# Kernel tuning notes

Measured on AMD Instinct MI355X. Metric: run time of the kernel, lower is better.

Reference implementation:

```python
import jax, jax.numpy as jnp
import numpy as np

B, NPTS = 32, 2048          # batch, raw points per cloud
G, M = 128, 32              # num_group (FPS centers), group_size (KNN)
C, DEPTH, H = 384, 12, 8    # trans_dim, depth, num_heads
HD = C // H                 # head_dim = 48, divisible by 6 for 3-axis RoPE
MLP = 4 * C
CLS = 40
THETA = 100.0


def _ln(x, g, b):
    m = x.mean(-1, keepdims=True)
    v = ((x - m) ** 2).mean(-1, keepdims=True)
    return (x - m) * jax.lax.rsqrt(v + 1e-5) * g + b


def _rot_pairs(x, cos, sin):
    # rotate consecutive (even, odd) pairs of the last dim by angle arrays
    x2 = x.reshape(x.shape[:-1] + (-1, 2))
    xr, xi = x2[..., 0], x2[..., 1]
    return jnp.stack([xr * cos - xi * sin, xr * sin + xi * cos], -1).reshape(x.shape)


def _fps(pts, n):
    # farthest point sampling, first point = index 0
    Bb, N, _ = pts.shape

    def step(carry, _):
        dist, last = carry
        lp = jnp.take_along_axis(pts, last[:, None, None], axis=1)  # (B,1,3)
        dist = jnp.minimum(dist, jnp.sum((pts - lp) ** 2, -1))
        nxt = jnp.argmax(dist, -1).astype(jnp.int32)
        return (dist, nxt), last

    init = (jnp.full((Bb, N), 1e10, pts.dtype), jnp.zeros((Bb,), jnp.int32))
    _, idxs = jax.lax.scan(step, init, None, length=n)
    return idxs.T  # (B, n)


def forward(pts, enc_w1, enc_b1, enc_g1, enc_be1, enc_w2, enc_b2,
            enc_w3, enc_b3, enc_g2, enc_be2, enc_w4, enc_b4,
            cls_token, cls_pos,
            ln1_g, ln1_b, qkv_w, givens_theta, proj_w, proj_b,
            ln2_g, ln2_b, fc1_w, fc1_b, fc2_w, fc2_b,
            norm_g, norm_b,
            hw1, hb1, hg1, hbe1, hw2, hb2, hg2, hbe2, hw3, hb3):
    # ---- Group divider: FPS centers + KNN neighborhoods ----
    cidx = _fps(pts, G)
    center = jnp.take_along_axis(pts, cidx[:, :, None], axis=1)          # (B,G,3)
    d2 = jnp.sum((center[:, :, None, :] - pts[:, None, :, :]) ** 2, -1)  # (B,G,N)
    _, kidx = jax.lax.top_k(-d2, M)                                      # (B,G,M)
    neigh = jax.vmap(lambda p, i: p[i])(pts, kidx) - center[:, :, None, :]

    # ---- mini-PointNet encoder (BN in eval mode: running mean 0, var 1) ----
    x = neigh.reshape(B * G, M, 3)
    f = jax.nn.relu((x @ enc_w1.T + enc_b1) * enc_g1 + enc_be1)          # (BG,M,128)
    f = f @ enc_w2.T + enc_b2                                            # (BG,M,256)
    fg = jnp.max(f, 1, keepdims=True)
    f = jnp.concatenate([jnp.broadcast_to(fg, f.shape), f], -1)          # (BG,M,512)
    f = jax.nn.relu((f @ enc_w3.T + enc_b3) * enc_g2 + enc_be2)
    f = f @ enc_w4.T + enc_b4                                            # (BG,M,C)
    tok = jnp.max(f, 1).reshape(B, G, C)

    # ---- 3-axis axial RoPE frequencies from group centers ----
    nfr = HD // 6
    fr = 1.0 / (THETA ** (jnp.arange(nfr, dtype=pts.dtype) * 2.0 / (HD // 3)))
    ang = (center[..., None] * fr).reshape(B, G, 3 * nfr)                # (B,G,HD/2)
    pcos, psin = jnp.cos(ang)[:, None], jnp.sin(ang)[:, None]            # (B,1,G,HD/2)

    # ---- tokens: [CLS | groups] ----
    x = jnp.concatenate([jnp.broadcast_to(cls_token + cls_pos, (B, 1, C)), tok], 1)
    N = G + 1
    scale = HD ** -0.5

    for i in range(DEPTH):
        h = _ln(x, ln1_g[i], ln1_b[i])
        qkv = (h @ qkv_w[i].T).reshape(B, N, 3, H, HD).transpose(2, 0, 3, 1, 4)
        q, k, v = qkv[0], qkv[1], qkv[2]                                 # (B,H,N,HD)
        # learnable Givens rotation (per-head block-diagonal pair rotations)
        gcos = jnp.cos(givens_theta[i])[None, :, None]                   # (1,H,1,HD/2)
        gsin = jnp.sin(givens_theta[i])[None, :, None]
        q = _rot_pairs(q, gcos, gsin)
        k = _rot_pairs(k, gcos, gsin)
        # positional RoPE on non-CLS tokens only
        q = jnp.concatenate([q[:, :, :1], _rot_pairs(q[:, :, 1:], pcos, psin)], 2)
        k = jnp.concatenate([k[:, :, :1], _rot_pairs(k[:, :, 1:], pcos, psin)], 2)
        attn = jax.nn.softmax(jnp.einsum('bhqd,bhkd->bhqk', q, k) * scale, -1)
        o = jnp.einsum('bhqk,bhkd->bhqd', attn, v).transpose(0, 2, 1, 3).reshape(B, N, C)
        x = x + o @ proj_w[i].T + proj_b[i]
        h = _ln(x, ln2_g[i], ln2_b[i])
        x = x + jax.nn.gelu(h @ fc1_w[i].T + fc1_b[i], approximate=False) @ fc2_w[i].T + fc2_b[i]

    x = _ln(x, norm_g, norm_b)
    feat = jnp.concatenate([x[:, 0], jnp.max(x[:, 1:], 1)], -1)          # (B,2C)
    hfe = jax.nn.relu((feat @ hw1.T + hb1) * hg1 + hbe1)
    hfe = jax.nn.relu((hfe @ hw2.T + hb2) * hg2 + hbe2)
    return hfe @ hw3.T + hb3                                             # (B,CLS)


def setup_inputs() -> dict:
    key = jax.random.key(0)
    ks = iter(jax.random.split(key, 64))
    nrm = lambda *s: jax.random.normal(next(ks), s, jnp.float32) * 0.02
    d = dict(
        pts=jax.random.normal(next(ks), (B, NPTS, 3), jnp.float32),
        enc_w1=nrm(128, 3), enc_b1=jnp.zeros(128), enc_g1=jnp.ones(128), enc_be1=jnp.zeros(128),
        enc_w2=nrm(256, 128), enc_b2=jnp.zeros(256),
        enc_w3=nrm(512, 512), enc_b3=jnp.zeros(512), enc_g2=jnp.ones(512), enc_be2=jnp.zeros(512),
        enc_w4=nrm(C, 512), enc_b4=jnp.zeros(C),
        cls_token=nrm(1, 1, C), cls_pos=nrm(1, 1, C),
        ln1_g=jnp.ones((DEPTH, C)), ln1_b=jnp.zeros((DEPTH, C)),
        qkv_w=nrm(DEPTH, 3 * C, C), givens_theta=nrm(DEPTH, H, HD // 2),
        proj_w=nrm(DEPTH, C, C), proj_b=jnp.zeros((DEPTH, C)),
        ln2_g=jnp.ones((DEPTH, C)), ln2_b=jnp.zeros((DEPTH, C)),
        fc1_w=nrm(DEPTH, MLP, C), fc1_b=jnp.zeros((DEPTH, MLP)),
        fc2_w=nrm(DEPTH, C, MLP), fc2_b=jnp.zeros((DEPTH, C)),
        norm_g=jnp.ones(C), norm_b=jnp.zeros(C),
        hw1=nrm(256, 2 * C), hb1=jnp.zeros(256), hg1=jnp.ones(256), hbe1=jnp.zeros(256),
        hw2=nrm(256, 256), hb2=jnp.zeros(256), hg2=jnp.ones(256), hbe2=jnp.zeros(256),
        hw3=nrm(CLS, 256), hb3=jnp.zeros(CLS),
    )
    return d


def reference(pts, enc_w1, enc_b1, enc_g1, enc_be1, enc_w2, enc_b2,
              enc_w3, enc_b3, enc_g2, enc_be2, enc_w4, enc_b4,
              cls_token, cls_pos,
              ln1_g, ln1_b, qkv_w, givens_theta, proj_w, proj_b,
              ln2_g, ln2_b, fc1_w, fc1_b, fc2_w, fc2_b,
              norm_g, norm_b,
              hw1, hb1, hg1, hbe1, hw2, hb2, hg2, hbe2, hw3, hb3):
    return forward(pts, enc_w1, enc_b1, enc_g1, enc_be1, enc_w2, enc_b2,
                   enc_w3, enc_b3, enc_g2, enc_be2, enc_w4, enc_b4,
                   cls_token, cls_pos,
                   ln1_g, ln1_b, qkv_w, givens_theta, proj_w, proj_b,
                   ln2_g, ln2_b, fc1_w, fc1_b, fc2_w, fc2_b,
                   norm_g, norm_b,
                   hw1, hb1, hg1, hbe1, hw2, hb2, hg2, hbe2, hw3, hb3)
```

## Files before the change

kernel.cpp:

```cpp
#include <hip/hip_runtime.h>
#include <math.h>

constexpr int kB   = 32;
constexpr int kN   = 2048;
constexpr int kG   = 128;
constexpr int kM   = 32;
constexpr int kC   = 384;
constexpr int kH   = 8;
constexpr int kHD  = 48;
constexpr int kNT  = 129;
constexpr int kMLP = 1536;
constexpr int kRows = kB * kNT;
constexpr int kGC  = 512;
constexpr int kRC  = kGC * kM;

typedef __attribute__((ext_vector_type(8))) short bf16x8;
typedef __attribute__((ext_vector_type(4))) float f32x4;

__device__ __forceinline__ unsigned short f2bf(float x) {
  unsigned u = __float_as_uint(x);
  unsigned r = (u + 0x7fffu + ((u >> 16) & 1u)) >> 16;
  return (unsigned short)r;
}
__device__ __forceinline__ float bf2f(unsigned short u) {
  return __uint_as_float(((unsigned)u) << 16);
}

__global__ __launch_bounds__(64) void fps_kernel(
    const float* __restrict__ pts, float* __restrict__ center)
{
  #pragma clang fp contract(off)
  __shared__ float sx[kN], sy[kN], sz[kN];
  const int b = blockIdx.x, lane = threadIdx.x;
  const float* P = pts + (size_t)b * kN * 3;
  float rx[32], ry[32], rz[32], rd[32];
  const int base = lane * 32;
  #pragma unroll
  for (int j = 0; j < 32; ++j) {
    int i = base + j;
    float x = P[3*i], y = P[3*i+1], z = P[3*i+2];
    rx[j] = x; ry[j] = y; rz[j] = z; rd[j] = 1e10f;
    sx[i] = x; sy[i] = y; sz[i] = z;
  }
  __syncthreads();
  int last = 0;
  float* cb = center + (size_t)b * kG * 3;
  for (int it = 0; it < kG; ++it) {
    float lx = sx[last], ly = sy[last], lz = sz[last];
    if (lane == 0) { cb[3*it] = lx; cb[3*it+1] = ly; cb[3*it+2] = lz; }
    float bestv = -1.0f; int besti = kN;
    #pragma unroll
    for (int j = 0; j < 32; ++j) {
      float dx = rx[j]-lx, dy = ry[j]-ly, dz = rz[j]-lz;
      float d = (dx*dx + dy*dy) + dz*dz;
      float nd = fminf(rd[j], d);
      rd[j] = nd;
      if (nd > bestv) { bestv = nd; besti = base + j; }
    }
    #pragma unroll
    for (int off = 1; off < 64; off <<= 1) {
      float vv = __shfl_xor(bestv, off);
      int   ii = __shfl_xor(besti, off);
      if (vv > bestv || (vv == bestv && ii < besti)) { bestv = vv; besti = ii; }
    }
    last = besti;
  }
}

__global__ void rope_kernel(const float* __restrict__ center,
                            float* __restrict__ pcs, float* __restrict__ psn)
{
  int idx = blockIdx.x*256 + threadIdx.x;
  if (idx >= kB*kG*24) return;
  int p  = idx % 24;
  int bg = idx / 24;
  int axis = p >> 3, j = p & 7;
  float e  = (float)(2*j) / 16.0f;
  float fr = 1.0f / powf(100.0f, e);
  float ang = center[(size_t)bg*3 + axis] * fr;
  pcs[idx] = cosf(ang);
  psn[idx] = sinf(ang);
}

__global__ __launch_bounds__(256) void knn_kernel(
    const float* __restrict__ pts, const float* __restrict__ center,
    float* __restrict__ neigh)
{
  #pragma clang fp contract(off)
  __shared__ float d2s[kN];
  __shared__ float rv[4];
  __shared__ int   ri[4];
  const int t = threadIdx.x;
  const int bg = blockIdx.x;
  const int b = bg >> 7;
  const float* P = pts + (size_t)b * kN * 3;
  const float cx = center[(size_t)bg*3+0];
  const float cy = center[(size_t)bg*3+1];
  const float cz = center[(size_t)bg*3+2];
  for (int i = t; i < kN; i += 256) {
    float dx = cx - P[3*i], dy = cy - P[3*i+1], dz = cz - P[3*i+2];
    d2s[i] = (dx*dx + dy*dy) + dz*dz;
  }
  __syncthreads();
  for (int m = 0; m < kM; ++m) {
    float bestv = 3.0e38f; int besti = kN;
    for (int i = t; i < kN; i += 256) {
      float v = d2s[i];
      if (v < bestv || (v == bestv && i < besti)) { bestv = v; besti = i; }
    }
    #pragma unroll
    for (int off = 32; off > 0; off >>= 1) {
      float vv = __shfl_down(bestv, off);
      int   ii = __shfl_down(besti, off);
      if (vv < bestv || (vv == bestv && ii < besti)) { bestv = vv; besti = ii; }
    }
    if ((t & 63) == 0) { rv[t>>6] = bestv; ri[t>>6] = besti; }
    __syncthreads();
    if (t == 0) {
      float bv = rv[0]; int bi = ri[0];
      for (int w = 1; w < 4; ++w)
        if (rv[w] < bv || (rv[w] == bv && ri[w] < bi)) { bv = rv[w]; bi = ri[w]; }
      d2s[bi] = 3.0e38f;
      float* o = neigh + ((size_t)bg*kM + m)*3;
      o[0] = P[3*bi+0] - cx; o[1] = P[3*bi+1] - cy; o[2] = P[3*bi+2] - cz;
    }
    __syncthreads();
  }
}

__global__ __launch_bounds__(256) void enc1_kernel(
    const float* __restrict__ neighC,
    const float* __restrict__ w1, const float* __restrict__ b1,
    const float* __restrict__ g1, const float* __restrict__ be1,
    unsigned short* __restrict__ f1c)
{
  const int t = threadIdx.x;
  const int r = blockIdx.x*2 + (t >> 7);
  const int c = t & 127;
  const float* nr = neighC + (size_t)r*3;
  float x0 = nr[0], x1 = nr[1], x2 = nr[2];
  float s = x0*w1[3*c] + x1*w1[3*c+1] + x2*w1[3*c+2] + b1[c];
  float v = fmaxf(s*g1[c] + be1[c], 0.0f);
  f1c[(size_t)r*128 + c] = f2bf(v);
}

__global__ __launch_bounds__(256) void pool2_kernel(
    const unsigned short* __restrict__ f2c, unsigned short* __restrict__ fgc)
{
  const int g = blockIdx.x, c = threadIdx.x;
  float mx = -3.0e38f;
  #pragma unroll 8
  for (int m = 0; m < kM; ++m)
    mx = fmaxf(mx, bf2f(f2c[((size_t)g*kM + m)*256 + c]));
  fgc[(size_t)g*256 + c] = f2bf(mx);
}

template <int EPI, int FM, int FN>
__global__ __launch_bounds__(256) void mgemm_kernel(
    const unsigned short* __restrict__ A, int lda,
    const float* __restrict__ B, int ldb,
    void* __restrict__ Cv,
    const float* __restrict__ bias,
    const float* __restrict__ aux,
    const float* __restrict__ gsc, const float* __restrict__ bsc,
    int Mm, int Nn, int Kk,
    float* __restrict__ poolOut, int poolG0)
{
  constexpr int BM = FM*32, BN = FN*32;
  __shared__ unsigned short As[BM][72];
  __shared__ unsigned short Bs[BN][72];
  const int t = threadIdx.x;
  const int m0 = blockIdx.x * BM;
  const int n0 = blockIdx.y * BN;
  const int w = t >> 6, lane = t & 63;
  const int wm = w >> 1, wn = w & 1;
  const int lr = lane & 15;
  const int lk = (lane >> 4) * 8;
  const int srow = t >> 3;
  const int skseg = (t & 7) * 8;
  f32x4 acc[FM][FN] = {};
  for (int k0 = 0; k0 < Kk; k0 += 64) {
    #pragma unroll
    for (int p = 0; p < BM/32; ++p) {
      int r = p*32 + srow;
      int gr = m0 + r;
      bf16x8 av = {};
      if (gr < Mm) av = *(const bf16x8*)(A + (size_t)gr*lda + k0 + skseg);
      *(bf16x8*)(&As[r][skseg]) = av;
    }
    #pragma unroll
    for (int p = 0; p < BN/32; ++p) {
      int r = p*32 + srow;
      const float* bp = B + (size_t)(n0 + r)*ldb + k0 + skseg;
      float4 b0 = *(const float4*)(bp);
      float4 b1 = *(const float4*)(bp + 4);
      bf16x8 bv;
      bv[0] = (short)f2bf(b0.x); bv[1] = (short)f2bf(b0.y);
      bv[2] = (short)f2bf(b0.z); bv[3] = (short)f2bf(b0.w);
      bv[4] = (short)f2bf(b1.x); bv[5] = (short)f2bf(b1.y);
      bv[6] = (short)f2bf(b1.z); bv[7] = (short)f2bf(b1.w);
      *(bf16x8*)(&Bs[r][skseg]) = bv;
    }
    __syncthreads();
    #pragma unroll
    for (int kk = 0; kk < 64; kk += 32) {
      bf16x8 af[FM], bf[FN];
      #pragma unroll
      for (int i = 0; i < FM; ++i)
        af[i] = *(const bf16x8*)(&As[wm*(FM*16) + i*16 + lr][kk + lk]);
      #pragma unroll
      for (int i = 0; i < FN; ++i)
        bf[i] = *(const bf16x8*)(&Bs[wn*(FN*16) + i*16 + lr][kk + lk]);
      #pragma unroll
      for (int i = 0; i < FM; ++i)
        #pragma unroll
        for (int j = 0; j < FN; ++j)
          acc[i][j] = __builtin_amdgcn_mfma_f32_16x16x32_bf16(af[i], bf[j], acc[i][j], 0, 0, 0);
    }
    __syncthreads();
  }

  if constexpr (EPI == 4) {
    #pragma unroll
    for (int ni = 0; ni < FN; ++ni) {
      int cc = n0 + wn*(FN*16) + ni*16 + lr;
      float mx = -3.0e38f;
      #pragma unroll
      for (int mi = 0; mi < FM; ++mi)
        #pragma unroll
        for (int j = 0; j < 4; ++j)
          mx = fmaxf(mx, acc[mi][ni][j]);
      mx = fmaxf(mx, __shfl_xor(mx, 16));
      mx = fmaxf(mx, __shfl_xor(mx, 32));
      if ((lane >> 4) == 0) {
        int ggl = poolG0 + (m0 >> 5) + wm;
        int b = ggl >> 7, g = ggl & 127;
        poolOut[((size_t)b*kNT + 1 + g)*kC + cc] = mx + bias[cc];
      }
    }
    return;
  }

  #pragma unroll
  for (int mi = 0; mi < FM; ++mi) {
    #pragma unroll
    for (int j = 0; j < 4; ++j) {
      int r = m0 + wm*(FM*16) + mi*16 + (lane >> 4)*4 + j;
      if (r < Mm) {
        #pragma unroll
        for (int ni = 0; ni < FN; ++ni) {
          int cc = n0 + wn*(FN*16) + ni*16 + lr;
          float v = acc[mi][ni][j];
          size_t o = (size_t)r*Nn + cc;
          if constexpr (EPI == 0) {
            ((unsigned short*)Cv)[o] = f2bf(v);
          } else if constexpr (EPI == 1) {
            ((unsigned short*)Cv)[o] = f2bf(v + bias[cc]);
          } else if constexpr (EPI == 2) {
            ((float*)Cv)[o] = v + bias[cc];
          } else if constexpr (EPI == 3) {
            float u = (v + aux[(size_t)(r >> 5)*Nn + cc])*gsc[cc] + bsc[cc];
            ((unsigned short*)Cv)[o] = f2bf(fmaxf(u, 0.0f));
          } else if constexpr (EPI == 5) {
            ((float*)Cv)[o] = aux[o] + v + bias[cc];
          } else {
            float u = v + bias[cc];
            ((unsigned short*)Cv)[o] = f2bf(0.5f*u*(1.0f + erff(u*0.70710678118654752440f)));
          }
        }
      }
    }
  }
}

__global__ void cls_kernel(const float* __restrict__ ct, const float* __restrict__ cp,
                           float* __restrict__ x)
{
  int idx = blockIdx.x*256 + threadIdx.x;
  if (idx >= kB*kC) return;
  int b = idx / kC, c = idx % kC;
  x[(size_t)b*kNT*kC + c] = ct[c] + cp[c];
}

template <int OUTBF>
__global__ __launch_bounds__(256) void ln_kernel(
    const float* __restrict__ in, void* __restrict__ outv,
    const float* __restrict__ g, const float* __restrict__ bb)
{
  const int t = threadIdx.x;
  const int lane = t & 63;
  const int row = blockIdx.x*4 + (t >> 6);
  const float* p = in + (size_t)row*kC;
  float v[6];
  #pragma unroll
  for (int k = 0; k < 6; ++k) v[k] = p[k*64 + lane];
  float s = 0.f;
  #pragma unroll
  for (int k = 0; k < 6; ++k) s += v[k];
  #pragma unroll
  for (int off = 1; off < 64; off <<= 1) s += __shfl_xor(s, off);
  float mean = s / 384.0f;
  float vs = 0.f;
  #pragma unroll
  for (int k = 0; k < 6; ++k) { float d = v[k]-mean; vs += d*d; }
  #pragma unroll
  for (int off = 1; off < 64; off <<= 1) vs += __shfl_xor(vs, off);
  float r = rsqrtf(vs / 384.0f + 1e-5f);
  #pragma unroll
  for (int k = 0; k < 6; ++k) {
    int c = k*64 + lane;
    float o = (v[k]-mean)*r*g[c] + bb[c];
    if constexpr (OUTBF) ((unsigned short*)outv)[(size_t)row*kC + c] = f2bf(o);
    else                 ((float*)outv)[(size_t)row*kC + c] = o;
  }
}

__global__ __launch_bounds__(512) void attn_kernel(
    const unsigned short* __restrict__ qkv, const float* __restrict__ pcs,
    const float* __restrict__ psn, const float* __restrict__ gth,
    unsigned short* __restrict__ o)
{
  __shared__ float qs[kNT][kHD];
  __shared__ float ks[kNT][kHD];
  __shared__ float vls[kNT][kHD];
  __shared__ float gcs[24], gss[24];
  __shared__ float ps[8][132];
  const int t = threadIdx.x;
  const int bh = blockIdx.x;
  const int b = bh >> 3, hh = bh & 7;
  if (t < 24) { float th = gth[hh*24 + t]; gcs[t] = cosf(th); gss[t] = sinf(th); }
  __syncthreads();
  for (int idx = t; idx < kNT*24; idx += 512) {
    int n = idx / 24, p = idx % 24;
    const unsigned short* base = qkv + ((size_t)(b*kNT + n))*1152 + hh*kHD + 2*p;
    float q0 = bf2f(base[0]),   q1 = bf2f(base[1]);
    float k0 = bf2f(base[384]), k1 = bf2f(base[385]);
    float v0 = bf2f(base[768]), v1 = bf2f(base[769]);
    float cg = gcs[p], sg = gss[p];
    float qr = q0*cg - q1*sg, qi = q0*sg + q1*cg;
    float kr = k0*cg - k1*sg, ki = k0*sg + k1*cg;
    if (n > 0) {
      size_t pi = ((size_t)b*kG + (n-1))*24 + p;
      float pc = pcs[pi], pv = psn[pi];
      float tq = qr*pc - qi*pv; qi = qr*pv + qi*pc; qr = tq;
      float tk = kr*pc - ki*pv; ki = kr*pv + ki*pc; kr = tk;
    }
    qs[n][2*p] = qr; qs[n][2*p+1] = qi;
    ks[n][2*p] = kr; ks[n][2*p+1] = ki;
    vls[n][2*p] = v0; vls[n][2*p+1] = v1;
  }
  __syncthreads();
  const int lane = t & 63, w = t >> 6;
  for (int r = w; r < kNT; r += 8) {
    float4 q[12];
    #pragma unroll
    for (int d = 0; d < 12; ++d) q[d] = *(const float4*)(&qs[r][d*4]);
    float sv[3];
    float mx = -3.0e38f;
    #pragma unroll
    for (int ji = 0; ji < 3; ++ji) {
      int j = ji*64 + lane;
      float s = -3.0e38f;
      if (j < kNT) {
        float a0 = 0.f, a1 = 0.f;
        #pragma unroll
        for (int d = 0; d < 12; d += 2) {
          float4 k0v = *(const float4*)(&ks[j][d*4]);
          float4 k1v = *(const float4*)(&ks[j][d*4+4]);
          a0 += q[d].x*k0v.x + q[d].y*k0v.y + q[d].z*k0v.z + q[d].w*k0v.w;
          a1 += q[d+1].x*k1v.x + q[d+1].y*k1v.y + q[d+1].z*k1v.z + q[d+1].w*k1v.w;
        }
        s = (a0 + a1) * 0.14433756729740643f;
      }
      sv[ji] = s;
      mx = fmaxf(mx, s);
    }
    #pragma unroll
    for (int off = 1; off < 64; off <<= 1) mx = fmaxf(mx, __shfl_xor(mx, off));
    float sum = 0.f;
    #pragma unroll
    for (int ji = 0; ji < 3; ++ji) {
      int j = ji*64 + lane;
      if (j < kNT) { float e = expf(sv[ji] - mx); ps[w][j] = e; sum += e; }
    }
    #pragma unroll
    for (int off = 1; off < 64; off <<= 1) sum += __shfl_xor(sum, off);
    if (lane < kHD) {
      float ac0 = 0.f, ac1 = 0.f, ac2 = 0.f, ac3 = 0.f;
      for (int j4 = 0; j4 < 128; j4 += 16) {
        float4 p0 = *(const float4*)(&ps[w][j4]);
        float4 p1 = *(const float4*)(&ps[w][j4+4]);
        float4 p2 = *(const float4*)(&ps[w][j4+8]);
        float4 p3 = *(const float4*)(&ps[w][j4+12]);
        ac0 += p0.x*vls[j4+0][lane] + p0.y*vls[j4+1][lane]
             + p0.z*vls[j4+2][lane] + p0.w*vls[j4+3][lane];
        ac1 += p1.x*vls[j4+4][lane] + p1.y*vls[j4+5][lane]
             + p1.z*vls[j4+6][lane] + p1.w*vls[j4+7][lane];
        ac2 += p2.x*vls[j4+8][lane] + p2.y*vls[j4+9][lane]
             + p2.z*vls[j4+10][lane] + p2.w*vls[j4+11][lane];
        ac3 += p3.x*vls[j4+12][lane] + p3.y*vls[j4+13][lane]
             + p3.z*vls[j4+14][lane] + p3.w*vls[j4+15][lane];
      }
      float accv = ((ac0 + ac1) + (ac2 + ac3)) + ps[w][128]*vls[128][lane];
      o[((size_t)(b*kNT + r))*kC + hh*kHD + lane] = f2bf(accv / sum);
    }
  }
}

__global__ __launch_bounds__(256) void head_kernel(
    const float* __restrict__ xf,
    const float* __restrict__ hw1, const float* __restrict__ hb1,
    const float* __restrict__ hg1, const float* __restrict__ hbe1,
    const float* __restrict__ hw2, const float* __restrict__ hb2,
    const float* __restrict__ hg2, const float* __restrict__ hbe2,
    const float* __restrict__ hw3, const float* __restrict__ hb3,
    float* __restrict__ out)
{
  __shared__ float f[768];
  __shared__ float h1[256], h2[256];
  const int t = threadIdx.x;
  const int b = blockIdx.x;
  const float* xb = xf + (size_t)b*kNT*kC;
  for (int c = t; c < kC; c += 256) {
    f[c] = xb[c];
    float mx = -3.0e38f;
    for (int n = 1; n < kNT; ++n) mx = fmaxf(mx, xb[(size_t)n*kC + c]);
    f[kC + c] = mx;
  }
  __syncthreads();
  {
    float acc = hb1[t];
    for (int k = 0; k < 768; k += 4) {
      float4 wv = *(const float4*)(hw1 + (size_t)t*768 + k);
      float4 fv = *(const float4*)(&f[k]);
      acc += fv.x*wv.x + fv.y*wv.y + fv.z*wv.z + fv.w*wv.w;
    }
    h1[t] = fmaxf(acc*hg1[t] + hbe1[t], 0.0f);
  }
  __syncthreads();
  {
    float acc = hb2[t];
    for (int k = 0; k < 256; k += 4) {
      float4 wv = *(const float4*)(hw2 + (size_t)t*256 + k);
      float4 fv = *(const float4*)(&h1[k]);
      acc += fv.x*wv.x + fv.y*wv.y + fv.z*wv.z + fv.w*wv.w;
    }
    h2[t] = fmaxf(acc*hg2[t] + hbe2[t], 0.0f);
  }
  __syncthreads();
  if (t < 40) {
    float acc = hb3[t];
    for (int k = 0; k < 256; k += 4) {
      float4 wv = *(const float4*)(hw3 + (size_t)t*256 + k);
      float4 fv = *(const float4*)(&h2[k]);
      acc += fv.x*wv.x + fv.y*wv.y + fv.z*wv.z + fv.w*wv.w;
    }
    out[(size_t)b*40 + t] = acc;
  }
}

extern "C" void kernel_launch(void* const* d_in, const int* in_sizes, int n_in,
                              void* d_out, int out_size, void* d_ws, size_t ws_size,
                              hipStream_t stream) {
  const float* pts     = (const float*)d_in[0];
  const float* enc_w1  = (const float*)d_in[1];
  const float* enc_b1  = (const float*)d_in[2];
  const float* enc_g1  = (const float*)d_in[3];
  const float* enc_be1 = (const float*)d_in[4];
  const float* enc_w2  = (const float*)d_in[5];
  const float* enc_b2  = (const float*)d_in[6];
  const float* enc_w3  = (const float*)d_in[7];
  const float* enc_b3  = (const float*)d_in[8];
  const float* enc_g2  = (const float*)d_in[9];
  const float* enc_be2 = (const float*)d_in[10];
  const float* enc_w4  = (const float*)d_in[11];
  const float* enc_b4  = (const float*)d_in[12];
  const float* cls_tok = (const float*)d_in[13];
  const float* cls_pos = (const float*)d_in[14];
  const float* ln1_g   = (const float*)d_in[15];
  const float* ln1_b   = (const float*)d_in[16];
  const float* qkv_w   = (const float*)d_in[17];
  const float* givens  = (const float*)d_in[18];
  const float* proj_w  = (const float*)d_in[19];
  const float* proj_b  = (const float*)d_in[20];
  const float* ln2_g   = (const float*)d_in[21];
  const float* ln2_b   = (const float*)d_in[22];
  const float* fc1_w   = (const float*)d_in[23];
  const float* fc1_b   = (const float*)d_in[24];
  const float* fc2_w   = (const float*)d_in[25];
  const float* fc2_b   = (const float*)d_in[26];
  const float* norm_g  = (const float*)d_in[27];
  const float* norm_b  = (const float*)d_in[28];
  const float* hw1     = (const float*)d_in[29];
  const float* hb1     = (const float*)d_in[30];
  const float* hg1     = (const float*)d_in[31];
  const float* hbe1    = (const float*)d_in[32];
  const float* hw2     = (const float*)d_in[33];
  const float* hb2     = (const float*)d_in[34];
  const float* hg2     = (const float*)d_in[35];
  const float* hbe2    = (const float*)d_in[36];
  const float* hw3     = (const float*)d_in[37];
  const float* hb3     = (const float*)d_in[38];

  char* wsb = (char*)d_ws;
  size_t off = 0;
  float* center = (float*)(wsb + off); off += (size_t)kB*kG*3*4;
  float* pcs    = (float*)(wsb + off); off += (size_t)kB*kG*24*4;
  float* psn    = (float*)(wsb + off); off += (size_t)kB*kG*24*4;
  float* neigh  = (float*)(wsb + off); off += (size_t)kB*kG*kM*3*4;
  float* xbuf   = (float*)(wsb + off); off += (size_t)kRows*kC*4;
  char* scratch = wsb + off;
  unsigned short* f1c   = (unsigned short*)(scratch);
  unsigned short* f2c   = (unsigned short*)(scratch + 4194304);
  unsigned short* fgc   = (unsigned short*)(scratch + 4194304 + 8388608);
  float*          basec = (float*)(scratch + 4194304 + 8388608 + 262144);
  unsigned short* f3c   = (unsigned short*)(scratch + 4194304 + 8388608 + 262144 + 1048576);
  unsigned short* hbuf   = (unsigned short*)(scratch);
  unsigned short* qkvb   = (unsigned short*)(scratch + 3170304);
  unsigned short* attnob = (unsigned short*)(scratch + 3170304 + 9510912);
  unsigned short* mlpb   = (unsigned short*)(scratch + 3170304 + 9510912 + 3170304);
  float*          flnb   = (float*)(scratch + 3170304);

  fps_kernel<<<kB, 64, 0, stream>>>(pts, center);
  rope_kernel<<<(kB*kG*24 + 255)/256, 256, 0, stream>>>(center, pcs, psn);
  knn_kernel<<<kB*kG, 256, 0, stream>>>(pts, center, neigh);

  for (int c = 0; c < 8; ++c) {
    const float* nc = neigh + (size_t)c*kRC*3;
    enc1_kernel<<<kRC/2, 256, 0, stream>>>(nc, enc_w1, enc_b1, enc_g1, enc_be1, f1c);
    mgemm_kernel<1,2,2><<<dim3(kRC/64, 4), 256, 0, stream>>>(
        f1c, 128, enc_w2, 128, f2c, enc_b2, nullptr, nullptr, nullptr,
        kRC, 256, 128, nullptr, 0);
    pool2_kernel<<<kGC, 256, 0, stream>>>(f2c, fgc);
    mgemm_kernel<2,2,2><<<dim3(kGC/64, 8), 256, 0, stream>>>(
        fgc, 256, enc_w3, 512, basec, enc_b3, nullptr, nullptr, nullptr,
        kGC, 512, 256, nullptr, 0);
    mgemm_kernel<3,2,2><<<dim3(kRC/64, 8), 256, 0, stream>>>(
        f2c, 256, enc_w3 + 256, 512, f3c, nullptr, basec, enc_g2, enc_be2,
        kRC, 512, 256, nullptr, 0);
    mgemm_kernel<4,2,2><<<dim3(kRC/64, 6), 256, 0, stream>>>(
        f3c, 512, enc_w4, 512, nullptr, enc_b4, nullptr, nullptr, nullptr,
        kRC, 384, 512, xbuf, c*kGC);
  }
  cls_kernel<<<(kB*kC + 255)/256, 256, 0, stream>>>(cls_tok, cls_pos, xbuf);

  const int lnGrid = kRows/4;
  for (int l = 0; l < 12; ++l) {
    ln_kernel<1><<<lnGrid, 256, 0, stream>>>(xbuf, hbuf, ln1_g + l*kC, ln1_b + l*kC);
    mgemm_kernel<0,2,2><<<dim3(65, 18), 256, 0, stream>>>(
        hbuf, kC, qkv_w + (size_t)l*1152*kC, kC, qkvb, nullptr, nullptr, nullptr, nullptr,
        kRows, 1152, kC, nullptr, 0);
    attn_kernel<<<kB*kH, 512, 0, stream>>>(qkvb, pcs, psn, givens + (size_t)l*kH*24, attnob);
    mgemm_kernel<5,2,2><<<dim3(65, 6), 256, 0, stream>>>(
        attnob, kC, proj_w + (size_t)l*kC*kC, kC, xbuf, proj_b + l*kC, xbuf, nullptr, nullptr,
        kRows, kC, kC, nullptr, 0);
    ln_kernel<1><<<lnGrid, 256, 0, stream>>>(xbuf, hbuf, ln2_g + l*kC, ln2_b + l*kC);
    mgemm_kernel<6,2,2><<<dim3(65, 24), 256, 0, stream>>>(
        hbuf, kC, fc1_w + (size_t)l*kMLP*kC, kC, mlpb, fc1_b + l*kMLP, nullptr, nullptr, nullptr,
        kRows, kMLP, kC, nullptr, 0);
    mgemm_kernel<5,2,2><<<dim3(65, 6), 256, 0, stream>>>(
        mlpb, kMLP, fc2_w + (size_t)l*kC*kMLP, kMLP, xbuf, fc2_b + l*kC, xbuf, nullptr, nullptr,
        kRows, kC, kMLP, nullptr, 0);
  }
  ln_kernel<0><<<lnGrid, 256, 0, stream>>>(xbuf, flnb, norm_g, norm_b);
  head_kernel<<<kB, 256, 0, stream>>>(flnb,
      hw1, hb1, hg1, hbe1, hw2, hb2, hg2, hbe2, hw3, hb3, (float*)d_out);
}
```

Before: 2.595 ms.

## Pre-convert GEMM weights to bf16 and rewrite KNN as wave-per-center register selection

Adds kernels that convert the encoder and per-layer transformer weights from fp32 to bf16 once into workspace, so the GEMM B-tile load reads bf16 directly instead of converting fp32 on every tile. The KNN kernel is restructured so each wavefront handles one center. Each lane keeps 32 distances in registers and block-wide barriers are replaced with a pure shuffle argmin, with points staged in padded shared memory. This adds extra conversion launches per layer and higher register use in KNN. The workspace layout is also reshuffled to alias the MLP buffer with the QKV region.

```diff
diff --git a/kernel.cpp b/kernel.cpp
--- a/kernel.cpp
+++ b/kernel.cpp
@@ -87,45 +87,81 @@
     float* __restrict__ neigh)
 {
   #pragma clang fp contract(off)
-  __shared__ float d2s[kN];
-  __shared__ float rv[4];
-  __shared__ int   ri[4];
+  __shared__ float sx[kN + kN/32], sy[kN + kN/32], sz[kN + kN/32];
   const int t = threadIdx.x;
-  const int bg = blockIdx.x;
-  const int b = bg >> 7;
+  const int lane = t & 63, w = t >> 6;
+  const int blk = blockIdx.x;
+  const int b = blk >> 5;
   const float* P = pts + (size_t)b * kN * 3;
+  for (int i = t; i < kN; i += 256) {
+    int ii = i + (i >> 5);
+    sx[ii] = P[3*i]; sy[ii] = P[3*i+1]; sz[ii] = P[3*i+2];
+  }
+  __syncthreads();
+  const int bg = b*kG + (blk & 31)*4 + w;
   const float cx = center[(size_t)bg*3+0];
   const float cy = center[(size_t)bg*3+1];
   const float cz = center[(size_t)bg*3+2];
-  for (int i = t; i < kN; i += 256) {
-    float dx = cx - P[3*i], dy = cy - P[3*i+1], dz = cz - P[3*i+2];
-    d2s[i] = (dx*dx + dy*dy) + dz*dz;
-  }
-  __syncthreads();
+  float rd[32];
+  const int base = lane * 32;
+  #pragma unroll
+  for (int j = 0; j < 32; ++j) {
+    int is = lane*33 + j;
+    float dx = cx - sx[is], dy = cy - sy[is], dz = cz - sz[is];
+    rd[j] = (dx*dx + dy*dy) + dz*dz;
+  }
+  float* ob = neigh + (size_t)bg * kM * 3;
+  int lastWin = -1;
   for (int m = 0; m < kM; ++m) {
     float bestv = 3.0e38f; int besti = kN;
-    for (int i = t; i < kN; i += 256) {
-      float v = d2s[i];
-      if (v < bestv || (v == bestv && i < besti)) { bestv = v; besti = i; }
-    }
-    #pragma unroll
-    for (int off = 32; off > 0; off >>= 1) {
-      float vv = __shfl_down(bestv, off);
-      int   ii = __shfl_down(besti, off);
-      if (vv < bestv || (vv == bestv && ii < besti)) { bestv = vv; besti = ii; }
-    }
-    if ((t & 63) == 0) { rv[t>>6] = bestv; ri[t>>6] = besti; }
-    __syncthreads();
-    if (t == 0) {
-      float bv = rv[0]; int bi = ri[0];
-      for (int w = 1; w < 4; ++w)
-        if (rv[w] < bv || (rv[w] == bv && ri[w] < bi)) { bv = rv[w]; bi = ri[w]; }
-      d2s[bi] = 3.0e38f;
-      float* o = neigh + ((size_t)bg*kM + m)*3;
-      o[0] = P[3*bi+0] - cx; o[1] = P[3*bi+1] - cy; o[2] = P[3*bi+2] - cz;
-    }
-    __syncthreads();
-  }
+    #pragma unroll
+    for (int j = 0; j < 32; ++j) {
+      float v = rd[j];
+      if (base + j == lastWin) v = 3.0e38f;
+      rd[j] = v;
+      if (v < bestv) { bestv = v; besti = base + j; }
+    }
+    #pragma unroll
+    for (int off = 1; off < 64; off <<= 1) {
+      float vv = __shfl_xor(bestv, off);
+      int   i2 = __shfl_xor(besti, off);
+      if (vv < bestv || (vv == bestv && i2 < besti)) { bestv = vv; besti = i2; }
+    }
+    lastWin = besti;
+    if (lane == 0) {
+      int is = besti + (besti >> 5);
+      ob[3*m+0] = sx[is] - cx; ob[3*m+1] = sy[is] - cy; ob[3*m+2] = sz[is] - cz;
+    }
+  }
+}
+
+__global__ void wcvt_kernel(const float* __restrict__ s,
+                            unsigned short* __restrict__ d, int n)
+{
+  int i = (blockIdx.x*256 + threadIdx.x)*8;
+  if (i >= n) return;
+  float4 a = *(const float4*)(s + i), b = *(const float4*)(s + i + 4);
+  bf16x8 v;
+  v[0]=(short)f2bf(a.x); v[1]=(short)f2bf(a.y); v[2]=(short)f2bf(a.z); v[3]=(short)f2bf(a.w);
+  v[4]=(short)f2bf(b.x); v[5]=(short)f2bf(b.y); v[6]=(short)f2bf(b.z); v[7]=(short)f2bf(b.w);
+  *(bf16x8*)(d + i) = v;
+}
+
+__global__ void wcvt4_kernel(const float* __restrict__ q, const float* __restrict__ p,
+                             const float* __restrict__ f1, const float* __restrict__ f2,
+                             unsigned short* __restrict__ d)
+{
+  int i = (blockIdx.x*256 + threadIdx.x)*8;
+  const float* s; int lo;
+  if (i < 442368)       { s = q;  lo = i; }
+  else if (i < 589824)  { s = p;  lo = i - 442368; }
+  else if (i < 1179648) { s = f1; lo = i - 589824; }
+  else                  { s = f2; lo = i - 1179648; }
+  float4 a = *(const float4*)(s + lo), b = *(const float4*)(s + lo + 4);
+  bf16x8 v;
+  v[0]=(short)f2bf(a.x); v[1]=(short)f2bf(a.y); v[2]=(short)f2bf(a.z); v[3]=(short)f2bf(a.w);
+  v[4]=(short)f2bf(b.x); v[5]=(short)f2bf(b.y); v[6]=(short)f2bf(b.z); v[7]=(short)f2bf(b.w);
+  *(bf16x8*)(d + i) = v;
 }
 
 __global__ __launch_bounds__(256) void enc1_kernel(
@@ -158,7 +194,7 @@
 template <int EPI, int FM, int FN>
 __global__ __launch_bounds__(256) void mgemm_kernel(
     const unsigned short* __restrict__ A, int lda,
-    const float* __restrict__ B, int ldb,
+    const unsigned short* __restrict__ Bb, int ldb,
     void* __restrict__ Cv,
     const float* __restrict__ bias,
     const float* __restrict__ aux,
@@ -191,14 +227,7 @@
     #pragma unroll
     for (int p = 0; p < BN/32; ++p) {
       int r = p*32 + srow;
-      const float* bp = B + (size_t)(n0 + r)*ldb + k0 + skseg;
-      float4 b0 = *(const float4*)(bp);
-      float4 b1 = *(const float4*)(bp + 4);
-      bf16x8 bv;
-      bv[0] = (short)f2bf(b0.x); bv[1] = (short)f2bf(b0.y);
-      bv[2] = (short)f2bf(b0.z); bv[3] = (short)f2bf(b0.w);
-      bv[4] = (short)f2bf(b1.x); bv[5] = (short)f2bf(b1.y);
-      bv[6] = (short)f2bf(b1.z); bv[7] = (short)f2bf(b1.w);
+      bf16x8 bv = *(const bf16x8*)(Bb + (size_t)(n0 + r)*ldb + k0 + skseg);
       *(bf16x8*)(&Bs[r][skseg]) = bv;
     }
     __syncthreads();
@@ -509,57 +538,74 @@
   float* psn    = (float*)(wsb + off); off += (size_t)kB*kG*24*4;
   float* neigh  = (float*)(wsb + off); off += (size_t)kB*kG*kM*3*4;
   float* xbuf   = (float*)(wsb + off); off += (size_t)kRows*kC*4;
+  unsigned short* encwb = (unsigned short*)(wsb + off); off += 491520ull*2;
+  unsigned short* wlbf  = (unsigned short*)(wsb + off); off += 1769472ull*2;
   char* scratch = wsb + off;
+  unsigned short* f3c   = (unsigned short*)(scratch);
   unsigned short* f1c   = (unsigned short*)(scratch);
-  unsigned short* f2c   = (unsigned short*)(scratch + 4194304);
-  unsigned short* fgc   = (unsigned short*)(scratch + 4194304 + 8388608);
-  float*          basec = (float*)(scratch + 4194304 + 8388608 + 262144);
-  unsigned short* f3c   = (unsigned short*)(scratch + 4194304 + 8388608 + 262144 + 1048576);
+  unsigned short* f2c   = (unsigned short*)(scratch + 16777216);
+  unsigned short* fgc   = (unsigned short*)(scratch + 16777216 + 8388608);
+  float*          basec = (float*)(scratch + 16777216 + 8388608 + 262144);
   unsigned short* hbuf   = (unsigned short*)(scratch);
   unsigned short* qkvb   = (unsigned short*)(scratch + 3170304);
   unsigned short* attnob = (unsigned short*)(scratch + 3170304 + 9510912);
-  unsigned short* mlpb   = (unsigned short*)(scratch + 3170304 + 9510912 + 3170304);
+  unsigned short* mlpb   = (unsigned short*)(scratch + 3170304);
   float*          flnb   = (float*)(scratch + 3170304);
+
+  const unsigned short* encw2 = encwb;
+  const unsigned short* encw3 = encwb + 32768;
+  const unsigned short* encw4 = encwb + 32768 + 262144;
 
   fps_kernel<<<kB, 64, 0, stream>>>(pts, center);
   rope_kernel<<<(kB*kG*24 + 255)/256, 256, 0, stream>>>(center, pcs, psn);
-  knn_kernel<<<kB*kG, 256, 0, stream>>>(pts, center, neigh);
+  knn_kernel<<<kB*kG/4, 256, 0, stream>>>(pts, center, neigh);
+
+  wcvt_kernel<<<32768/8/256, 256, 0, stream>>>(enc_w2, (unsigned short*)encw2, 32768);
+  wcvt_kernel<<<262144/8/256, 256, 0, stream>>>(enc_w3, (unsigned short*)encw3, 262144);
+  wcvt_kernel<<<196608/8/256, 256, 0, stream>>>(enc_w4, (unsigned short*)encw4, 196608);
 
   for (int c = 0; c < 8; ++c) {
     const float* nc = neigh + (size_t)c*kRC*3;
     enc1_kernel<<<kRC/2, 256, 0, stream>>>(nc, enc_w1, enc_b1, enc_g1, enc_be1, f1c);
     mgemm_kernel<1,2,2><<<dim3(kRC/64, 4), 256, 0, stream>>>(
-        f1c, 128, enc_w2, 128, f2c, enc_b2, nullptr, nullptr, nullptr,
+        f1c, 128, encw2, 128, f2c, enc_b2, nullptr, nullptr, nullptr,
         kRC, 256, 128, nullptr, 0);
     pool2_kernel<<<kGC, 256, 0, stream>>>(f2c, fgc);
     mgemm_kernel<2,2,2><<<dim3(kGC/64, 8), 256, 0, stream>>>(
-        fgc, 256, enc_w3, 512, basec, enc_b3, nullptr, nullptr, nullptr,
+        fgc, 256, encw3, 512, basec, enc_b3, nullptr, nullptr, nullptr,
         kGC, 512, 256, nullptr, 0);
     mgemm_kernel<3,2,2><<<dim3(kRC/64, 8), 256, 0, stream>>>(
-        f2c, 256, enc_w3 + 256, 512, f3c, nullptr, basec, enc_g2, enc_be2,
+        f2c, 256, encw3 + 256, 512, f3c, nullptr, basec, enc_g2, enc_be2,
         kRC, 512, 256, nullptr, 0);
     mgemm_kernel<4,2,2><<<dim3(kRC/64, 6), 256, 0, stream>>>(
-        f3c, 512, enc_w4, 512, nullptr, enc_b4, nullptr, nullptr, nullptr,
+        f3c, 512, encw4, 512, nullptr, enc_b4, nullptr, nullptr, nullptr,
         kRC, 384, 512, xbuf, c*kGC);
   }
   cls_kernel<<<(kB*kC + 255)/256, 256, 0, stream>>>(cls_tok, cls_pos, xbuf);
 
+  const unsigned short* wq = wlbf;
+  const unsigned short* wp = wlbf + 442368;
+  const unsigned short* w1f = wlbf + 589824;
+  const unsigned short* w2f = wlbf + 1179648;
   const int lnGrid = kRows/4;
   for (int l = 0; l < 12; ++l) {
+    wcvt4_kernel<<<864, 256, 0, stream>>>(
+        qkv_w + (size_t)l*442368, proj_w + (size_t)l*147456,
+        fc1_w + (size_t)l*589824, fc2_w + (size_t)l*589824, wlbf);
     ln_kernel<1><<<lnGrid, 256, 0, stream>>>(xbuf, hbuf, ln1_g + l*kC, ln1_b + l*kC);
     mgemm_kernel<0,2,2><<<dim3(65, 18), 256, 0, stream>>>(
-        hbuf, kC, qkv_w + (size_t)l*1152*kC, kC, qkvb, nullptr, nullptr, nullptr, nullptr,
+        hbuf, kC, wq, kC, qkvb, nullptr, nullptr, nullptr, nullptr,
         kRows, 1152, kC, nullptr, 0);
     attn_kernel<<<kB*kH, 512, 0, stream>>>(qkvb, pcs, psn, givens + (size_t)l*kH*24, attnob);
     mgemm_kernel<5,2,2><<<dim3(65, 6), 256, 0, stream>>>(
-        attnob, kC, proj_w + (size_t)l*kC*kC, kC, xbuf, proj_b + l*kC, xbuf, nullptr, nullptr,
+        attnob, kC, wp, kC, xbuf, proj_b + l*kC, xbuf, nullptr, nullptr,
         kRows, kC, kC, nullptr, 0);
     ln_kernel<1><<<lnGrid, 256, 0, stream>>>(xbuf, hbuf, ln2_g + l*kC, ln2_b + l*kC);
     mgemm_kernel<6,2,2><<<dim3(65, 24), 256, 0, stream>>>(
-        hbuf, kC, fc1_w + (size_t)l*kMLP*kC, kC, mlpb, fc1_b + l*kMLP, nullptr, nullptr, nullptr,
+        hbuf, kC, w1f, kC, mlpb, fc1_b + l*kMLP, nullptr, nullptr, nullptr,
         kRows, kMLP, kC, nullptr, 0);
     mgemm_kernel<5,2,2><<<dim3(65, 6), 256, 0, stream>>>(
-        mlpb, kMLP, fc2_w + (size_t)l*kC*kMLP, kMLP, xbuf, fc2_b + l*kC, xbuf, nullptr, nullptr,
+        mlpb, kMLP, w2f, kMLP, xbuf, fc2_b + l*kC, xbuf, nullptr, nullptr,
         kRows, kC, kMLP, nullptr, 0);
   }
   ln_kernel<0><<<lnGrid, 256, 0, stream>>>(xbuf, flnb, norm_g, norm_b);
```

Result: faster. 2.415 ms (-7.0%).
